# Performance work log

Hardware: AMD Instinct MI355X
Metric: run time of the kernel (lower is better)

## Reference

```python
import jax, jax.numpy as jnp
import numpy as np

D_MODEL = 1024
NUM_HEADS = 16
HEAD_DIM = D_MODEL // NUM_HEADS


def setup_inputs() -> dict:
    key = jax.random.key(0)
    k_x, k_wqkv, k_bqkv, k_wo, k_bo = jax.random.split(key, 5)
    B, T = 4, 2048
    s = 1.0 / np.sqrt(D_MODEL)
    return {
        "x": jax.random.normal(k_x, (B, T, D_MODEL), dtype=jnp.float32),
        "w_qkv": jax.random.uniform(k_wqkv, (D_MODEL, 3 * D_MODEL), jnp.float32, -s, s),
        "b_qkv": jax.random.uniform(k_bqkv, (3 * D_MODEL,), jnp.float32, -s, s),
        "w_out": jax.random.uniform(k_wo, (D_MODEL, D_MODEL), jnp.float32, -s, s),
        "b_out": jax.random.uniform(k_bo, (D_MODEL,), jnp.float32, -s, s),
    }


def reference(x, w_qkv, b_qkv, w_out, b_out):
    B, T, _ = x.shape
    H, Dh = NUM_HEADS, HEAD_DIM
    scale = Dh ** -0.5
    qkv = x @ w_qkv + b_qkv                       # [B,T,3D]
    qkv = qkv.reshape(B, T, 3, H, Dh)
    q = jnp.transpose(qkv[:, :, 0], (0, 2, 1, 3))  # [B,H,T,Dh]
    k = jnp.transpose(qkv[:, :, 1], (0, 2, 1, 3))
    v = jnp.transpose(qkv[:, :, 2], (0, 2, 1, 3))
    scores = jnp.einsum('bhqd,bhkd->bhqk', q, k) * scale
    causal = jnp.tril(jnp.ones((T, T), dtype=bool))
    scores = jnp.where(causal, scores, -jnp.inf)
    w = jax.nn.softmax(scores, axis=-1)
    out = jnp.einsum('bhqk,bhkd->bhqd', w, v)     # [B,H,T,Dh]
    out = jnp.transpose(out, (0, 2, 1, 3)).reshape(B, T, H * Dh)
    return out @ w_out + b_out
```

## Files before the change

### kernel.cpp

```cpp
#include <hip/hip_runtime.h>

typedef unsigned short u16;
typedef unsigned u32;
typedef float f32x4 __attribute__((ext_vector_type(4)));
typedef __bf16 bf16x8 __attribute__((ext_vector_type(8)));
typedef __bf16 bf16x2 __attribute__((ext_vector_type(2)));
typedef u32 u32x4 __attribute__((ext_vector_type(4)));
typedef u16 u16x4 __attribute__((ext_vector_type(4)));
typedef int i32x2 __attribute__((ext_vector_type(2)));

#define MFMA_16x16x32(a, b, c) __builtin_amdgcn_mfma_f32_16x16x32_bf16((a), (b), (c), 0, 0, 0)

#if __has_builtin(__builtin_amdgcn_exp2f)
#define EXP2(x) __builtin_amdgcn_exp2f(x)
#else
#define EXP2(x) exp2f(x)
#endif


__device__ __forceinline__ u16 f2bf(float f) {
  unsigned u = __builtin_bit_cast(unsigned, f);
  unsigned r = ((u >> 16) & 1u) + 0x7FFFu;
  return (u16)((u + r) >> 16);
}

__device__ __forceinline__ u32 pk2(float x, float y) {
  bf16x2 v = {(__bf16)x, (__bf16)y};
  return __builtin_bit_cast(u32, v);
}

__device__ __forceinline__ void gload16(const void* g, void* l) {
  __builtin_amdgcn_global_load_lds(
      (const __attribute__((address_space(1))) void*)g,
      (__attribute__((address_space(3))) void*)l, 16, 0, 0);
}



__global__ void cvt_to_bf16(const float* __restrict__ in, u16* __restrict__ out, int n) {
  const int s = blockIdx.x * 256 + threadIdx.x;
  if (s * 8 >= n) return;
  const int l = s & 63, f = (s >> 6) & 7, kb = (s >> 9) & 31, R = s >> 14;
  const int rr = ((f >> 2) << 6) + ((f & 3) << 4) + (l & 15);
  const int row = (R << 7) + rr;
  const int k = (kb << 5) + ((l >> 4) << 3);
  const float* src = in + (size_t)row * 1024 + k;
  const f32x4 a = *(const f32x4*)src;
  const f32x4 b = *(const f32x4*)(src + 4);
  u16x4 u0, u1;
#pragma unroll
  for (int j = 0; j < 4; ++j) { u0[j] = f2bf(a[j]); u1[j] = f2bf(b[j]); }
  *(u16x4*)(out + (size_t)s * 8) = u0;
  *(u16x4*)(out + (size_t)s * 8 + 4) = u1;
}

__global__ void transpose_cvt(const float* __restrict__ in, u16* __restrict__ out,
                              int rows, int cols) {
  __shared__ float t[64][65];
  const int rb = blockIdx.y * 64, cb = blockIdx.x * 64;
  for (int i = threadIdx.x; i < 4096; i += 256) {
    const int r = i >> 6, c = i & 63;
    t[r][c] = in[(size_t)(rb + r) * cols + cb + c];
  }
  __syncthreads();
  for (int u = threadIdx.x; u < 512; u += 256) {
    const int c = u >> 3, k8 = u & 7;
    const int nrow = cb + c;
    const int kg = rb + k8 * 8;
    const int R = nrow >> 7, rr = nrow & 127;
    const int fB = ((rr >> 6) << 2) + ((rr >> 4) & 3);
    const int kb = kg >> 5, koct = (kg >> 3) & 3;
    u16* dst = out + (((size_t)R * 32 + kb) * 8 + fB) * 512 + ((koct << 4) + (rr & 15)) * 8;
    u16x4 u0, u1;
#pragma unroll
    for (int j = 0; j < 4; ++j) {
      u0[j] = f2bf(t[k8 * 8 + j][c]);
      u1[j] = f2bf(t[k8 * 8 + 4 + j][c]);
    }
    *(u16x4*)dst = u0;
    *(u16x4*)(dst + 4) = u1;
  }
}

template <int EPI>
__global__ __launch_bounds__(256, 4) void gemm_bt(
    const u16* __restrict__ A, const u16* __restrict__ Bt, int K,
    const float* __restrict__ bias,
    u16* __restrict__ oq, u16* __restrict__ ok, u16* __restrict__ ov,
    float* __restrict__ of, int N, int nbx) {
  __shared__ __align__(16) u16 As[4096];
  __shared__ __align__(16) u16 Bs[4096];
  const int tid = threadIdx.x;
  const int lane = tid & 63, w = tid >> 6;
  const int g = lane >> 4, cc = lane & 15;
  const int wr = w >> 1, wc = w & 1;

  const int cpx = gridDim.x >> 3;
  const int bid = ((int)blockIdx.x & 7) * cpx + ((int)blockIdx.x >> 3);
  const int bx = bid % nbx, by = bid / nbx;

  const u16* pa = A + ((size_t)by * 256 + w) * 512 + lane * 8;
  const u16* pb = Bt + ((size_t)bx * 256 + w) * 512 + lane * 8;

  u16* la0 = &As[w * 512 + lane * 8];
  u16* la1 = &As[(w + 4) * 512 + lane * 8];
  u16* lb0 = &Bs[w * 512 + lane * 8];
  u16* lb1 = &Bs[(w + 4) * 512 + lane * 8];
  const u16* ard = &As[(wr * 4) * 512 + lane * 8];
  const u16* brd = &Bs[(wc * 4) * 512 + lane * 8];

  f32x4 acc[4][4] = {};

  const int nkb = K >> 5;
  for (int kb = 0; kb < nkb; ++kb) {
    const size_t o = (size_t)kb * 4096;
    gload16(pa + o, la0);
    gload16(pa + o + 2048, la1);
    gload16(pb + o, lb0);
    gload16(pb + o + 2048, lb1);
    __syncthreads();
    bf16x8 af[4], bf[4];
#pragma unroll
    for (int mi = 0; mi < 4; ++mi) af[mi] = *(const bf16x8*)(ard + mi * 512);
#pragma unroll
    for (int ni = 0; ni < 4; ++ni) bf[ni] = *(const bf16x8*)(brd + ni * 512);
    __builtin_amdgcn_s_setprio(1);
#pragma unroll
    for (int mi = 0; mi < 4; ++mi)
#pragma unroll
      for (int ni = 0; ni < 4; ++ni)
        acc[mi][ni] = MFMA_16x16x32(af[mi], bf[ni], acc[mi][ni]);
    __builtin_amdgcn_s_setprio(0);
    __syncthreads();
  }

  const int m00 = by * 128 + wr * 64 + 4 * g;
  const int n00 = bx * 128 + wc * 64;
#pragma unroll
  for (int ni = 0; ni < 4; ++ni) {
    const int n = n00 + ni * 16 + cc;
    const float bn = bias[n];
    if constexpr (EPI == 0) {
      const int which = n >> 10;
      const int d = n & 1023;
      const int h = d >> 6, dh = d & 63;
      const int dcf = dh >> 5, gf = (dh >> 3) & 3, e = dh & 7;
      const int niv = dh >> 4, ccv = dh & 15;
#pragma unroll
      for (int mi = 0; mi < 4; ++mi) {
        const int mb = m00 + mi * 16;
        const int b = mb >> 11, t0b = mb & 2047;
        const int bh2 = b * 16 + h;
        const int kt = t0b >> 7, tr = t0b & 127;
        if (which == 2) {
          const int kk0 = (tr & ~12) | ((tr & 4) << 1) | ((tr & 8) >> 1);
          const int ko = kk0 >> 5, gv = (kk0 >> 3) & 3, ev = kk0 & 7;
          u16x4 pk;
#pragma unroll
          for (int r = 0; r < 4; ++r) pk[r] = f2bf(acc[mi][ni][r] + bn);
          *(u16x4*)&ov[(((size_t)bh2 * 16 + kt) * 16 + ko * 4 + niv) * 512 +
                       ((gv << 4) + ccv) * 8 + ev] = pk;
        } else if (which == 1) {
          const int ki = tr >> 4;
          u16* dst = ok + (((size_t)bh2 * 16 + kt) * 16 + dcf * 8 + ki) * 512 +
                     ((gf << 4) + (tr & 15)) * 8 + e;
#pragma unroll
          for (int r = 0; r < 4; ++r) dst[r * 8] = f2bf(acc[mi][ni][r] + bn);
        } else {
          const int wf = tr >> 5, mif = (tr >> 4) & 1;
          u16* dst = oq + (((size_t)bh2 * 16 + kt) * 16 + wf * 4 + mif * 2 + dcf) * 512 +
                     ((gf << 4) + (tr & 15)) * 8 + e;
#pragma unroll
          for (int r = 0; r < 4; ++r) dst[r * 8] = f2bf(acc[mi][ni][r] + bn);
        }
      }
    } else {
#pragma unroll
      for (int mi = 0; mi < 4; ++mi) {
        const int m = m00 + mi * 16;
#pragma unroll
        for (int r = 0; r < 4; ++r) of[(size_t)(m + r) * N + n] = acc[mi][ni][r] + bn;
      }
    }
  }
}

__global__ __launch_bounds__(256, 4) void flash_attn(
    const u16* __restrict__ Qb, const u16* __restrict__ Kb,
    const u16* __restrict__ Vt, u16* __restrict__ Ob) {
  __shared__ __align__(16) u16 Ks[8192];
  __shared__ __align__(16) u16 Vs[8192];

  const int bid = blockIdx.x;
  const int tq4 = bid >> 6, t0 = tq4 & 3, ti = tq4 >> 2;
  const int qt = (ti == 0) ? 15 - t0 : (ti == 1) ? 8 + t0 : (ti == 2) ? 7 - t0 : t0;
  const int bh = bid & 63;
  const int tid = threadIdx.x;
  const int lane = tid & 63, w = tid >> 6;
  const int g = lane >> 4, cc = lane & 15;
  const int q0 = qt * 128 + w * 32;

  bf16x8 bq[2][2];
  {
    const u16* qp = Qb + (((size_t)bh * 16 + qt) * 16 + w * 4) * 512 + lane * 8;
#pragma unroll
    for (int mi = 0; mi < 2; ++mi)
#pragma unroll
      for (int dc = 0; dc < 2; ++dc)
        bq[mi][dc] = *(const bf16x8*)(qp + (mi * 2 + dc) * 512);
  }

  const char* kp = (const char*)Kb + (size_t)bh * 262144 + w * 1024 + lane * 16;
  const char* vp = (const char*)Vt + (size_t)bh * 262144 + w * 1024 + lane * 16;
  u16* kl[4];
  u16* vl[4];
#pragma unroll
  for (int i = 0; i < 4; ++i) {
    kl[i] = &Ks[(i * 4 + w) * 512 + lane * 8];
    vl[i] = &Vs[(i * 4 + w) * 512 + lane * 8];
  }
  const u16* krd = &Ks[lane * 8];
  const u16* vrd = &Vs[lane * 8];

  f32x4 acc[2][4] = {};
  float m_run[2] = {-1e30f, -1e30f};
  float l_run[2] = {0.f, 0.f};
  const float sc = 0.18033688011112042f;

  for (int kt = 0; kt <= qt; ++kt) {
    __syncthreads();
#pragma unroll
    for (int i = 0; i < 4; ++i) gload16(kp + i * 4096, kl[i]);
#pragma unroll
    for (int i = 0; i < 4; ++i) gload16(vp + i * 4096, vl[i]);
    kp += 16384;
    vp += 16384;
    __syncthreads();

#pragma unroll
    for (int mi = 0; mi < 2; ++mi) {
      f32x4 s[8] = {};
      __builtin_amdgcn_s_setprio(1);
#pragma unroll
      for (int dc = 0; dc < 2; ++dc) {
        const bf16x8 qf = bq[mi][dc];
#pragma unroll
        for (int ki = 0; ki < 8; ++ki) {
          const bf16x8 ak = *(const bf16x8*)(krd + (dc * 8 + ki) * 512);
          s[ki] = MFMA_16x16x32(ak, qf, s[ki]);
        }
      }
      __builtin_amdgcn_s_setprio(0);

      if (kt == qt) {
        const int qq = w * 32 + mi * 16 + cc;
#pragma unroll
        for (int ki = 0; ki < 8; ++ki) {
          const int kb_ = ki * 16 + 4 * g;
#pragma unroll
          for (int r = 0; r < 4; ++r)
            if (kb_ + r > qq) s[ki][r] = -1e30f;
        }
      }

      float mx = fmaxf(fmaxf(s[0][0], s[0][1]), fmaxf(s[0][2], s[0][3]));
#pragma unroll
      for (int ki = 1; ki < 8; ++ki)
        mx = fmaxf(mx, fmaxf(fmaxf(s[ki][0], s[ki][1]), fmaxf(s[ki][2], s[ki][3])));
      mx = fmaxf(mx, __shfl_xor(mx, 16));
      mx = fmaxf(mx, __shfl_xor(mx, 32));
      const float pm = mx * sc;

      if (!__all(pm - m_run[mi] <= 8.f)) {
        const float mn = fmaxf(m_run[mi], pm);
        const float sf = EXP2(m_run[mi] - mn);
        m_run[mi] = mn;
        l_run[mi] *= sf;
        float sfr[4];
#pragma unroll
        for (int r = 0; r < 4; ++r) sfr[r] = __shfl(sf, (lane & 48) + 4 * g + r);
#pragma unroll
        for (int ni = 0; ni < 4; ++ni)
#pragma unroll
          for (int r = 0; r < 4; ++r) acc[mi][ni][r] *= sfr[r];
      }
      const float mcur = m_run[mi];

      f32x4 rsv = {};
#pragma unroll
      for (int ko = 0; ko < 4; ++ko) {
        f32x4 pe, po;
#pragma unroll
        for (int r = 0; r < 4; ++r) {
          pe[r] = EXP2(__builtin_fmaf(s[2 * ko][r], sc, -mcur));
          po[r] = EXP2(__builtin_fmaf(s[2 * ko + 1][r], sc, -mcur));
        }
        rsv += pe;
        rsv += po;
        const u32 aw = pk2(pe[0], pe[1]), bw2 = pk2(pe[2], pe[3]);
        const u32 cw = pk2(po[0], po[1]), dw = pk2(po[2], po[3]);
#if __has_builtin(__builtin_amdgcn_permlane32_swap)
        const i32x2 s1 = __builtin_amdgcn_permlane32_swap((int)aw, (int)cw, false, false);
        const i32x2 s2 = __builtin_amdgcn_permlane32_swap((int)bw2, (int)dw, false, false);
        const u32x4 wv = {(u32)s1[0], (u32)s2[0], (u32)s1[1], (u32)s2[1]};
#else
        const bool lo2 = (g < 2);
        const u32 r_ac = __shfl_xor(lo2 ? cw : aw, 32);
        const u32 r_bd = __shfl_xor(lo2 ? dw : bw2, 32);
        const u32x4 wv = {lo2 ? aw : r_ac, lo2 ? bw2 : r_bd,
                          lo2 ? r_ac : cw, lo2 ? r_bd : dw};
#endif
        const bf16x8 pf = __builtin_bit_cast(bf16x8, wv);
        __builtin_amdgcn_s_setprio(1);
#pragma unroll
        for (int ni = 0; ni < 4; ++ni) {
          const bf16x8 bv = *(const bf16x8*)(vrd + (ko * 4 + ni) * 512);
          acc[mi][ni] = MFMA_16x16x32(pf, bv, acc[mi][ni]);
        }
        __builtin_amdgcn_s_setprio(0);
      }
      float rs = (rsv[0] + rsv[1]) + (rsv[2] + rsv[3]);
      rs += __shfl_xor(rs, 16);
      rs += __shfl_xor(rs, 32);
      l_run[mi] += rs;
    }
  }

  const int b = bh >> 4, h = bh & 15;
#pragma unroll
  for (int mi = 0; mi < 2; ++mi) {
    float inv[4];
#pragma unroll
    for (int r = 0; r < 4; ++r)
      inv[r] = 1.f / __shfl(l_run[mi], (lane & 48) + 4 * g + r);
#pragma unroll
    for (int ni = 0; ni < 4; ++ni) {
      const int d = h * 64 + ni * 16 + cc;
      const int kbA = d >> 5, koA = (d >> 3) & 3, eA = d & 7;
#pragma unroll
      for (int r = 0; r < 4; ++r) {
        const int tq = q0 + mi * 16 + 4 * g + r;
        const int row = b * 2048 + tq;
        const int R = row >> 7, rr = row & 127;
        const int fA = ((rr >> 6) << 2) + ((rr >> 4) & 3);
        Ob[(((size_t)R * 32 + kbA) * 8 + fA) * 512 + ((koA << 4) + (rr & 15)) * 8 + eA] =
            f2bf(acc[mi][ni][r] * inv[r]);
      }
    }
  }
}


extern "C" void kernel_launch(void* const* d_in, const int* in_sizes, int n_in,
                              void* d_out, int out_size, void* d_ws, size_t ws_size,
                              hipStream_t stream) {
  const float* x     = (const float*)d_in[0];
  const float* w_qkv = (const float*)d_in[1];
  const float* b_qkv = (const float*)d_in[2];
  const float* w_out = (const float*)d_in[3];
  const float* b_out = (const float*)d_in[4];
  float* out = (float*)d_out;
  char* ws = (char*)d_ws;

  u16* xb    = (u16*)(ws + 0);
  u16* wqkvT = (u16*)(ws + 16777216);
  u16* woutT = (u16*)(ws + 23068672);
  u16* qbuf  = (u16*)(ws + 25165824);
  u16* kbuf  = (u16*)(ws + 41943040);
  u16* vbuf  = (u16*)(ws + 58720256);

  cvt_to_bf16<<<4096, 256, 0, stream>>>(x, xb, 8388608);
  transpose_cvt<<<dim3(48, 16), 256, 0, stream>>>(w_qkv, wqkvT, 1024, 3072);
  transpose_cvt<<<dim3(16, 16), 256, 0, stream>>>(w_out, woutT, 1024, 1024);
  gemm_bt<0><<<24 * 64, 256, 0, stream>>>(xb, wqkvT, 1024, b_qkv,
                                          qbuf, kbuf, vbuf, nullptr, 3072, 24);
  flash_attn<<<1024, 256, 0, stream>>>(qbuf, kbuf, vbuf, xb);
  gemm_bt<1><<<8 * 64, 256, 0, stream>>>(xb, woutT, 1024, b_out,
                                         nullptr, nullptr, nullptr, out, 1024, 8);
}
```

Measured before the change: 172.1 us.

## Deepen GEMM K-step, register-prefetch K/V tiles, compute softmax row sums via MFMA

The GEMM now stages 64 K-elements per iteration with doubled LDS tiles, which halves the number of barrier pairs per output tile. The attention kernel preloads the next K/V tile into registers while the current tile is computed, so global load latency overlaps compute instead of the direct global-to-LDS loads used before. The softmax denominator is accumulated with an extra MFMA against a ones vector, replacing the VALU sums and cross-lane shuffles. The costs are higher LDS use in the GEMM, which may lower occupancy, more registers in attention, and denominator sums taken from bf16-rounded probabilities.

After: 220.9 us. +28.4%, slower.

```diff
diff --git a/kernel.cpp b/kernel.cpp
--- a/kernel.cpp
+++ b/kernel.cpp
@@ -88,8 +88,8 @@
     const float* __restrict__ bias,
     u16* __restrict__ oq, u16* __restrict__ ok, u16* __restrict__ ov,
     float* __restrict__ of, int N, int nbx) {
-  __shared__ __align__(16) u16 As[4096];
-  __shared__ __align__(16) u16 Bs[4096];
+  __shared__ __align__(16) u16 As[8192];
+  __shared__ __align__(16) u16 Bs[8192];
   const int tid = threadIdx.x;
   const int lane = tid & 63, w = tid >> 6;
   const int g = lane >> 4, cc = lane & 15;
@@ -103,34 +103,39 @@
   const u16* pb = Bt + ((size_t)bx * 256 + w) * 512 + lane * 8;
 
   u16* la0 = &As[w * 512 + lane * 8];
-  u16* la1 = &As[(w + 4) * 512 + lane * 8];
   u16* lb0 = &Bs[w * 512 + lane * 8];
-  u16* lb1 = &Bs[(w + 4) * 512 + lane * 8];
   const u16* ard = &As[(wr * 4) * 512 + lane * 8];
   const u16* brd = &Bs[(wc * 4) * 512 + lane * 8];
 
   f32x4 acc[4][4] = {};
 
-  const int nkb = K >> 5;
-  for (int kb = 0; kb < nkb; ++kb) {
-    const size_t o = (size_t)kb * 4096;
+  const int ns = K >> 6;
+  for (int s = 0; s < ns; ++s) {
+    const size_t o = (size_t)s * 8192;
     gload16(pa + o, la0);
-    gload16(pa + o + 2048, la1);
+    gload16(pa + o + 2048, la0 + 2048);
+    gload16(pa + o + 4096, la0 + 4096);
+    gload16(pa + o + 6144, la0 + 6144);
     gload16(pb + o, lb0);
-    gload16(pb + o + 2048, lb1);
+    gload16(pb + o + 2048, lb0 + 2048);
+    gload16(pb + o + 4096, lb0 + 4096);
+    gload16(pb + o + 6144, lb0 + 6144);
     __syncthreads();
-    bf16x8 af[4], bf[4];
-#pragma unroll
-    for (int mi = 0; mi < 4; ++mi) af[mi] = *(const bf16x8*)(ard + mi * 512);
-#pragma unroll
-    for (int ni = 0; ni < 4; ++ni) bf[ni] = *(const bf16x8*)(brd + ni * 512);
-    __builtin_amdgcn_s_setprio(1);
-#pragma unroll
-    for (int mi = 0; mi < 4; ++mi)
-#pragma unroll
-      for (int ni = 0; ni < 4; ++ni)
-        acc[mi][ni] = MFMA_16x16x32(af[mi], bf[ni], acc[mi][ni]);
-    __builtin_amdgcn_s_setprio(0);
+#pragma unroll
+    for (int kk = 0; kk < 2; ++kk) {
+      bf16x8 af[4], bf[4];
+#pragma unroll
+      for (int mi = 0; mi < 4; ++mi) af[mi] = *(const bf16x8*)(ard + kk * 4096 + mi * 512);
+#pragma unroll
+      for (int ni = 0; ni < 4; ++ni) bf[ni] = *(const bf16x8*)(brd + kk * 4096 + ni * 512);
+      __builtin_amdgcn_s_setprio(1);
+#pragma unroll
+      for (int mi = 0; mi < 4; ++mi)
+#pragma unroll
+        for (int ni = 0; ni < 4; ++ni)
+          acc[mi][ni] = MFMA_16x16x32(af[mi], bf[ni], acc[mi][ni]);
+      __builtin_amdgcn_s_setprio(0);
+    }
     __syncthreads();
   }
 
@@ -222,19 +227,39 @@
   const u16* krd = &Ks[lane * 8];
   const u16* vrd = &Vs[lane * 8];
 
+  const u32x4 ones_u = {0x3F803F80u, 0x3F803F80u, 0x3F803F80u, 0x3F803F80u};
+  const bf16x8 ones = __builtin_bit_cast(bf16x8, ones_u);
+
   f32x4 acc[2][4] = {};
+  f32x4 lsum[2] = {};
   float m_run[2] = {-1e30f, -1e30f};
-  float l_run[2] = {0.f, 0.f};
   const float sc = 0.18033688011112042f;
+
+  u32x4 kreg[4], vreg[4];
+#pragma unroll
+  for (int i = 0; i < 4; ++i) {
+    kreg[i] = *(const u32x4*)(kp + i * 4096);
+    vreg[i] = *(const u32x4*)(vp + i * 4096);
+  }
+  kp += 16384;
+  vp += 16384;
 
   for (int kt = 0; kt <= qt; ++kt) {
     __syncthreads();
 #pragma unroll
-    for (int i = 0; i < 4; ++i) gload16(kp + i * 4096, kl[i]);
-#pragma unroll
-    for (int i = 0; i < 4; ++i) gload16(vp + i * 4096, vl[i]);
-    kp += 16384;
-    vp += 16384;
+    for (int i = 0; i < 4; ++i) {
+      *(u32x4*)kl[i] = kreg[i];
+      *(u32x4*)vl[i] = vreg[i];
+    }
+    if (kt < qt) {
+#pragma unroll
+      for (int i = 0; i < 4; ++i) {
+        kreg[i] = *(const u32x4*)(kp + i * 4096);
+        vreg[i] = *(const u32x4*)(vp + i * 4096);
+      }
+      kp += 16384;
+      vp += 16384;
+    }
     __syncthreads();
 
 #pragma unroll
@@ -275,18 +300,18 @@
         const float mn = fmaxf(m_run[mi], pm);
         const float sf = EXP2(m_run[mi] - mn);
         m_run[mi] = mn;
-        l_run[mi] *= sf;
         float sfr[4];
 #pragma unroll
         for (int r = 0; r < 4; ++r) sfr[r] = __shfl(sf, (lane & 48) + 4 * g + r);
 #pragma unroll
+        for (int r = 0; r < 4; ++r) lsum[mi][r] *= sfr[r];
+#pragma unroll
         for (int ni = 0; ni < 4; ++ni)
 #pragma unroll
           for (int r = 0; r < 4; ++r) acc[mi][ni][r] *= sfr[r];
       }
       const float mcur = m_run[mi];
 
-      f32x4 rsv = {};
 #pragma unroll
       for (int ko = 0; ko < 4; ++ko) {
         f32x4 pe, po;
@@ -295,8 +320,6 @@
           pe[r] = EXP2(__builtin_fmaf(s[2 * ko][r], sc, -mcur));
           po[r] = EXP2(__builtin_fmaf(s[2 * ko + 1][r], sc, -mcur));
         }
-        rsv += pe;
-        rsv += po;
         const u32 aw = pk2(pe[0], pe[1]), bw2 = pk2(pe[2], pe[3]);
         const u32 cw = pk2(po[0], po[1]), dw = pk2(po[2], po[3]);
 #if __has_builtin(__builtin_amdgcn_permlane32_swap)
@@ -317,22 +340,18 @@
           const bf16x8 bv = *(const bf16x8*)(vrd + (ko * 4 + ni) * 512);
           acc[mi][ni] = MFMA_16x16x32(pf, bv, acc[mi][ni]);
         }
+        lsum[mi] = MFMA_16x16x32(pf, ones, lsum[mi]);
         __builtin_amdgcn_s_setprio(0);
       }
-      float rs = (rsv[0] + rsv[1]) + (rsv[2] + rsv[3]);
-      rs += __shfl_xor(rs, 16);
-      rs += __shfl_xor(rs, 32);
-      l_run[mi] += rs;
     }
   }
 
   const int b = bh >> 4, h = bh & 15;
 #pragma unroll
   for (int mi = 0; mi < 2; ++mi) {
-    float inv[4];
-#pragma unroll
-    for (int r = 0; r < 4; ++r)
-      inv[r] = 1.f / __shfl(l_run[mi], (lane & 48) + 4 * g + r);
+    f32x4 inv;
+#pragma unroll
+    for (int r = 0; r < 4; ++r) inv[r] = 1.f / lsum[mi][r];
 #pragma unroll
     for (int ni = 0; ni < 4; ++ni) {
       const int d = h * 64 + ni * 16 + cc;
```
